# Optimization experiments

Measured on AMD Instinct MI355X. Metric: run time of the kernel, lower is better.

The kernel has to match this reference:

```python
import jax, jax.numpy as jnp
import numpy as np

B, D = 1024, 512


def setup_inputs() -> dict:
    key = jax.random.key(0)
    k1, k2, k3 = jax.random.split(key, 3)
    x = jax.random.normal(k1, (B, D), dtype=jnp.float32)
    x_dot = jax.random.normal(k2, (B, D), dtype=jnp.float32)
    # linear score network weight: s(x) = x @ W^T  (scaled for sane magnitudes)
    W = jax.random.normal(k3, (D, D), dtype=jnp.float32) / np.sqrt(D).astype(np.float32)
    return {"x": x, "x_dot": x_dot, "W": W}


def reference(x, x_dot, W):
    # s(x): [b, d]
    s = x @ W.T
    d = x.shape[1]
    # g(x) = I + s s^T : [b, d, d]  (faithful to the original bmm formulation)
    G = jnp.eye(d, dtype=x.dtype)[None, :, :] + s[:, :, None] * s[:, None, :]
    # kinetic energy: x_dot^T G x_dot : [b]
    return jnp.einsum('bi,bij,bj->b', x_dot, G, x_dot)
```

## Files before the change

kernel.cpp:

```cpp
#include <hip/hip_runtime.h>

#define BB 1024
#define DD 512
#define BTILE 32
#define JTILE 128
#define ICH 64
#define NIC (DD / ICH)
#define NTP ((DD / JTILE) * NIC)
#define NNP (NIC * 4)

__global__ __launch_bounds__(256, 4) void stm_main_kernel(
    const float* __restrict__ x, const float* __restrict__ xdot,
    const float* __restrict__ W, float* __restrict__ ws_t) {
  __shared__ float xd_t[ICH][BTILE];
  __shared__ float w_s[ICH][JTILE];

  const int tid = threadIdx.x;
  const int b0 = blockIdx.x * BTILE;
  const int j0 = blockIdx.y * JTILE;
  const int i0 = blockIdx.z * ICH;
  const int tb = tid >> 5;
  const int tj = tid & 31;

  float nrm = 0.f;
  {
    const int row = tid & 31;
    const int f4 = tid >> 5;
    const float4* src = (const float4*)(xdot + (size_t)(b0 + row) * DD + i0);
#pragma unroll
    for (int p = 0; p < 2; ++p) {
      const int c4 = f4 + p * 8;
      float4 v = src[c4];
      nrm += v.x * v.x + v.y * v.y + v.z * v.z + v.w * v.w;
      const int c = c4 * 4;
      xd_t[c + 0][row] = v.x; xd_t[c + 1][row] = v.y;
      xd_t[c + 2][row] = v.z; xd_t[c + 3][row] = v.w;
    }
  }
  {
#pragma unroll
    for (int v = 0; v < 8; ++v) {
      const int f4 = tid + v * 256;
      const int ii = f4 >> 5, jj4 = f4 & 31;
      *((float4*)&w_s[ii][jj4 * 4]) =
          ((const float4*)(W + (size_t)(i0 + ii) * DD + j0))[jj4];
    }
  }

  if (blockIdx.y == 0) {
    nrm += __shfl_xor(nrm, 32);
    const int wv = tid >> 6, ln = tid & 63;
    if (ln < 32)
      ws_t[(size_t)(NTP + blockIdx.z * 4 + wv) * BB + b0 + ln] = nrm;
  }

  float4 xv[4];
#pragma unroll
  for (int r = 0; r < 4; ++r)
    xv[r] = ((const float4*)(x + (size_t)(b0 + tb * 4 + r) * DD + j0))[tj];

  __syncthreads();

  float acc[4][4] = {};
#pragma unroll
  for (int i = 0; i < ICH; ++i) {
    const float4 xd = *(const float4*)&xd_t[i][tb * 4];
    const float4 w  = *(const float4*)&w_s[i][tj * 4];
    acc[0][0] += xd.x * w.x; acc[0][1] += xd.x * w.y;
    acc[0][2] += xd.x * w.z; acc[0][3] += xd.x * w.w;
    acc[1][0] += xd.y * w.x; acc[1][1] += xd.y * w.y;
    acc[1][2] += xd.y * w.z; acc[1][3] += xd.y * w.w;
    acc[2][0] += xd.z * w.x; acc[2][1] += xd.z * w.y;
    acc[2][2] += xd.z * w.z; acc[2][3] += xd.z * w.w;
    acc[3][0] += xd.w * w.x; acc[3][1] += xd.w * w.y;
    acc[3][2] += xd.w * w.z; acc[3][3] += xd.w * w.w;
  }

  float tp[4];
#pragma unroll
  for (int r = 0; r < 4; ++r)
    tp[r] = acc[r][0] * xv[r].x + acc[r][1] * xv[r].y +
            acc[r][2] * xv[r].z + acc[r][3] * xv[r].w;
#pragma unroll
  for (int off = 16; off >= 1; off >>= 1) {
#pragma unroll
    for (int r = 0; r < 4; ++r) tp[r] += __shfl_xor(tp[r], off);
  }
  if (tj == 0) {
    const int p = blockIdx.y * NIC + blockIdx.z;
    *(float4*)(ws_t + (size_t)p * BB + b0 + tb * 4) =
        make_float4(tp[0], tp[1], tp[2], tp[3]);
  }
}

__global__ __launch_bounds__(256) void stm_final_kernel(
    const float* __restrict__ ws_t, float* __restrict__ out) {
  const int b = blockIdx.x * 256 + threadIdx.x;
  float t = 0.f, n = 0.f;
#pragma unroll
  for (int p = 0; p < NTP; ++p) t += ws_t[(size_t)p * BB + b];
#pragma unroll
  for (int p = 0; p < NNP; ++p) n += ws_t[(size_t)(NTP + p) * BB + b];
  out[b] = n + t * t;
}

extern "C" void kernel_launch(void* const* d_in, const int* in_sizes, int n_in,
                              void* d_out, int out_size, void* d_ws, size_t ws_size,
                              hipStream_t stream) {
  const float* x    = (const float*)d_in[0];
  const float* xdot = (const float*)d_in[1];
  const float* W    = (const float*)d_in[2];
  float* ws = (float*)d_ws;
  float* out = (float*)d_out;

  dim3 g1(BB / BTILE, DD / JTILE, NIC);
  stm_main_kernel<<<g1, 256, 0, stream>>>(x, xdot, W, ws);
  stm_final_kernel<<<BB / 256, 256, 0, stream>>>(ws, out);
}
```

Measured before the change: 69.01 us.

## Retile main kernel to 64-row batch tiles with 8x4 per-thread outputs

Changes the block tile from 32x128 over a 64-wide reduction chunk to 64x128 over a 32-wide chunk, so each thread accumulates 8 rows by 4 columns. This raises arithmetic intensity per shared-memory load and halves the W load per block, at the cost of twice as many partial sums for the final reduction kernel to read. The x loads move after the inner loop rather than being prefetched before the barrier, and each partial-sum slot now covers a larger batch range.

New measurement: 69.80 us. No clear change (+1.1%).

```diff
diff --git a/kernel.cpp b/kernel.cpp
--- a/kernel.cpp
+++ b/kernel.cpp
@@ -2,94 +2,93 @@
 
 #define BB 1024
 #define DD 512
-#define BTILE 32
-#define JTILE 128
-#define ICH 64
-#define NIC (DD / ICH)
-#define NTP ((DD / JTILE) * NIC)
+#define BT 64
+#define JT 128
+#define KT 32
+#define NIC (DD / KT)
+#define NTP ((DD / JT) * NIC)
 #define NNP (NIC * 4)
 
 __global__ __launch_bounds__(256, 4) void stm_main_kernel(
     const float* __restrict__ x, const float* __restrict__ xdot,
     const float* __restrict__ W, float* __restrict__ ws_t) {
-  __shared__ float xd_t[ICH][BTILE];
-  __shared__ float w_s[ICH][JTILE];
+  __shared__ float xd_t[KT][BT];
+  __shared__ float w_s[KT][JT];
 
   const int tid = threadIdx.x;
-  const int b0 = blockIdx.x * BTILE;
-  const int j0 = blockIdx.y * JTILE;
-  const int i0 = blockIdx.z * ICH;
+  const int b0 = blockIdx.x * BT;
+  const int j0 = blockIdx.y * JT;
+  const int i0 = blockIdx.z * KT;
   const int tb = tid >> 5;
   const int tj = tid & 31;
+  const int wv = tid >> 6, lane = tid & 63;
 
   float nrm = 0.f;
   {
-    const int row = tid & 31;
-    const int f4 = tid >> 5;
-    const float4* src = (const float4*)(xdot + (size_t)(b0 + row) * DD + i0);
+    const float* src = xdot + (size_t)(b0 + lane) * DD + i0;
 #pragma unroll
     for (int p = 0; p < 2; ++p) {
-      const int c4 = f4 + p * 8;
-      float4 v = src[c4];
+      const int c4 = wv + p * 4;
+      const float4 v = *(const float4*)(src + c4 * 4);
       nrm += v.x * v.x + v.y * v.y + v.z * v.z + v.w * v.w;
       const int c = c4 * 4;
-      xd_t[c + 0][row] = v.x; xd_t[c + 1][row] = v.y;
-      xd_t[c + 2][row] = v.z; xd_t[c + 3][row] = v.w;
+      xd_t[c + 0][lane] = v.x; xd_t[c + 1][lane] = v.y;
+      xd_t[c + 2][lane] = v.z; xd_t[c + 3][lane] = v.w;
     }
   }
-  {
 #pragma unroll
-    for (int v = 0; v < 8; ++v) {
-      const int f4 = tid + v * 256;
-      const int ii = f4 >> 5, jj4 = f4 & 31;
-      *((float4*)&w_s[ii][jj4 * 4]) =
-          ((const float4*)(W + (size_t)(i0 + ii) * DD + j0))[jj4];
-    }
+  for (int v = 0; v < 4; ++v) {
+    const int f4 = tid + v * 256;
+    const int ii = f4 >> 5, jj4 = f4 & 31;
+    *(float4*)&w_s[ii][jj4 * 4] =
+        *(const float4*)(W + (size_t)(i0 + ii) * DD + j0 + jj4 * 4);
+  }
+  if (blockIdx.y == 0)
+    ws_t[(size_t)(NTP + blockIdx.z * 4 + wv) * BB + b0 + lane] = nrm;
+  __syncthreads();
+
+  float acc[8][4] = {};
+#pragma unroll
+  for (int i = 0; i < KT; ++i) {
+    const float4 xlo = *(const float4*)&xd_t[i][tb * 8];
+    const float4 xhi = *(const float4*)&xd_t[i][tb * 8 + 4];
+    const float4 w   = *(const float4*)&w_s[i][tj * 4];
+    acc[0][0] += xlo.x * w.x; acc[0][1] += xlo.x * w.y;
+    acc[0][2] += xlo.x * w.z; acc[0][3] += xlo.x * w.w;
+    acc[1][0] += xlo.y * w.x; acc[1][1] += xlo.y * w.y;
+    acc[1][2] += xlo.y * w.z; acc[1][3] += xlo.y * w.w;
+    acc[2][0] += xlo.z * w.x; acc[2][1] += xlo.z * w.y;
+    acc[2][2] += xlo.z * w.z; acc[2][3] += xlo.z * w.w;
+    acc[3][0] += xlo.w * w.x; acc[3][1] += xlo.w * w.y;
+    acc[3][2] += xlo.w * w.z; acc[3][3] += xlo.w * w.w;
+    acc[4][0] += xhi.x * w.x; acc[4][1] += xhi.x * w.y;
+    acc[4][2] += xhi.x * w.z; acc[4][3] += xhi.x * w.w;
+    acc[5][0] += xhi.y * w.x; acc[5][1] += xhi.y * w.y;
+    acc[5][2] += xhi.y * w.z; acc[5][3] += xhi.y * w.w;
+    acc[6][0] += xhi.z * w.x; acc[6][1] += xhi.z * w.y;
+    acc[6][2] += xhi.z * w.z; acc[6][3] += xhi.z * w.w;
+    acc[7][0] += xhi.w * w.x; acc[7][1] += xhi.w * w.y;
+    acc[7][2] += xhi.w * w.z; acc[7][3] += xhi.w * w.w;
   }
 
-  if (blockIdx.y == 0) {
-    nrm += __shfl_xor(nrm, 32);
-    const int wv = tid >> 6, ln = tid & 63;
-    if (ln < 32)
-      ws_t[(size_t)(NTP + blockIdx.z * 4 + wv) * BB + b0 + ln] = nrm;
+  float tp[8];
+#pragma unroll
+  for (int r = 0; r < 8; ++r) {
+    const float4 xv =
+        *(const float4*)(x + (size_t)(b0 + tb * 8 + r) * DD + j0 + tj * 4);
+    tp[r] = acc[r][0] * xv.x + acc[r][1] * xv.y +
+            acc[r][2] * xv.z + acc[r][3] * xv.w;
   }
-
-  float4 xv[4];
-#pragma unroll
-  for (int r = 0; r < 4; ++r)
-    xv[r] = ((const float4*)(x + (size_t)(b0 + tb * 4 + r) * DD + j0))[tj];
-
-  __syncthreads();
-
-  float acc[4][4] = {};
-#pragma unroll
-  for (int i = 0; i < ICH; ++i) {
-    const float4 xd = *(const float4*)&xd_t[i][tb * 4];
-    const float4 w  = *(const float4*)&w_s[i][tj * 4];
-    acc[0][0] += xd.x * w.x; acc[0][1] += xd.x * w.y;
-    acc[0][2] += xd.x * w.z; acc[0][3] += xd.x * w.w;
-    acc[1][0] += xd.y * w.x; acc[1][1] += xd.y * w.y;
-    acc[1][2] += xd.y * w.z; acc[1][3] += xd.y * w.w;
-    acc[2][0] += xd.z * w.x; acc[2][1] += xd.z * w.y;
-    acc[2][2] += xd.z * w.z; acc[2][3] += xd.z * w.w;
-    acc[3][0] += xd.w * w.x; acc[3][1] += xd.w * w.y;
-    acc[3][2] += xd.w * w.z; acc[3][3] += xd.w * w.w;
-  }
-
-  float tp[4];
-#pragma unroll
-  for (int r = 0; r < 4; ++r)
-    tp[r] = acc[r][0] * xv[r].x + acc[r][1] * xv[r].y +
-            acc[r][2] * xv[r].z + acc[r][3] * xv[r].w;
 #pragma unroll
   for (int off = 16; off >= 1; off >>= 1) {
 #pragma unroll
-    for (int r = 0; r < 4; ++r) tp[r] += __shfl_xor(tp[r], off);
+    for (int r = 0; r < 8; ++r) tp[r] += __shfl_xor(tp[r], off);
   }
   if (tj == 0) {
     const int p = blockIdx.y * NIC + blockIdx.z;
-    *(float4*)(ws_t + (size_t)p * BB + b0 + tb * 4) =
-        make_float4(tp[0], tp[1], tp[2], tp[3]);
+    float* dst = ws_t + (size_t)p * BB + b0 + tb * 8;
+    *(float4*)(dst + 0) = make_float4(tp[0], tp[1], tp[2], tp[3]);
+    *(float4*)(dst + 4) = make_float4(tp[4], tp[5], tp[6], tp[7]);
   }
 }
 
@@ -113,7 +112,7 @@
   float* ws = (float*)d_ws;
   float* out = (float*)d_out;
 
-  dim3 g1(BB / BTILE, DD / JTILE, NIC);
+  dim3 g1(BB / BT, DD / JT, NIC);
   stm_main_kernel<<<g1, 256, 0, stream>>>(x, xdot, W, ws);
   stm_final_kernel<<<BB / 256, 256, 0, stream>>>(ws, out);
 }
```
